# Kernel tuning notes

Measured on AMD Instinct MI355X. Metric: run time of the kernel, lower is better.

The kernel has to match this reference:

```python
import jax, jax.numpy as jnp
import numpy as np

D_IN = 1024
D_OUT = 1024
BATCH = 4
SEQ = 2048


def setup_inputs() -> dict:
    key = jax.random.key(0)
    kx, kq, kk, kv = jax.random.split(key, 4)
    # nn.Linear default init: U(-1/sqrt(d_in), 1/sqrt(d_in)); exact dist irrelevant for a reference
    bound = 1.0 / np.sqrt(D_IN)
    x = jax.random.normal(kx, (BATCH, SEQ, D_IN), dtype=jnp.float32)
    W_query = jax.random.uniform(kq, (D_IN, D_OUT), dtype=jnp.float32, minval=-bound, maxval=bound)
    W_key = jax.random.uniform(kk, (D_IN, D_OUT), dtype=jnp.float32, minval=-bound, maxval=bound)
    W_value = jax.random.uniform(kv, (D_IN, D_OUT), dtype=jnp.float32, minval=-bound, maxval=bound)
    return {"x": x, "W_query": W_query, "W_key": W_key, "W_value": W_value}


def reference(x, W_query, W_key, W_value):
    # x: [b, s, d_in]; projections (qkv_bias=False)
    q = jnp.einsum("bsd,df->bsf", x, W_query)  # [b, s, d_out]
    k = jnp.einsum("bsd,df->bsf", x, W_key)
    v = jnp.einsum("bsd,df->bsf", x, W_value)

    scale = 1.0 / jnp.sqrt(jnp.asarray(k.shape[-1], dtype=x.dtype))
    scores = jnp.einsum("bqf,bkf->bqk", q, k) * scale  # [b, s, s]

    s = x.shape[1]
    causal = jnp.tril(jnp.ones((s, s), dtype=bool))  # True where allowed
    scores = jnp.where(causal[None, :, :], scores, -jnp.inf)

    weights = jax.nn.softmax(scores, axis=-1)
    # dropout_ratio=0.0 -> identity
    return jnp.einsum("bqk,bkf->bqf", weights, v)  # [b, s, d_out]
```

## Files before the change

### kernel.cpp

```cpp
#include <hip/hip_runtime.h>


typedef __bf16 bf16x8 __attribute__((ext_vector_type(8)));
typedef float f32x4 __attribute__((ext_vector_type(4)));

__device__ __forceinline__ unsigned short f2bf(float f) {
  unsigned int u = __builtin_bit_cast(unsigned int, f);
  u += 0x7FFFu + ((u >> 16) & 1u);
  return (unsigned short)(u >> 16);
}
__device__ __forceinline__ float bf2f(unsigned short h) {
  unsigned int u = ((unsigned int)h) << 16;
  return __builtin_bit_cast(float, u);
}

#define GLDS16(g, l)                                                                   \
  __builtin_amdgcn_global_load_lds((const __attribute__((address_space(1))) void*)(g), \
                                   (__attribute__((address_space(3))) void*)(l), 16, 0, 0)

__global__ __launch_bounds__(256) void k_cvt(const float* __restrict__ in,
                                             unsigned short* __restrict__ out, long n) {
  long i = ((long)blockIdx.x * 256 + threadIdx.x) * 8;
  if (i >= n) return;
  float4 a = *(const float4*)(in + i);
  float4 b = *(const float4*)(in + i + 4);
  uint4 o;
  o.x = (unsigned)f2bf(a.x) | ((unsigned)f2bf(a.y) << 16);
  o.y = (unsigned)f2bf(a.z) | ((unsigned)f2bf(a.w) << 16);
  o.z = (unsigned)f2bf(b.x) | ((unsigned)f2bf(b.y) << 16);
  o.w = (unsigned)f2bf(b.z) | ((unsigned)f2bf(b.w) << 16);
  *(uint4*)(out + i) = o;
}

__global__ void k_trans_w(const float* __restrict__ W0, const float* __restrict__ W1,
                          const float* __restrict__ W2, unsigned short* __restrict__ Wt, int D) {
  const float* W = blockIdx.z == 0 ? W0 : (blockIdx.z == 1 ? W1 : W2);
  unsigned short* out = Wt + (long)blockIdx.z * D * D;
  __shared__ float tile[32][33];
  int tx = threadIdx.x, ty = threadIdx.y;
  int bx = blockIdx.x * 32, by = blockIdx.y * 32;
#pragma unroll
  for (int j = 0; j < 4; ++j) tile[ty + j * 8][tx] = W[(long)(by + ty + j * 8) * D + bx + tx];
  __syncthreads();
#pragma unroll
  for (int j = 0; j < 4; ++j)
    out[(long)(bx + ty + j * 8) * D + by + tx] = f2bf(tile[tx][ty + j * 8]);
}

template <typename CT>
__global__ __launch_bounds__(512, 2) void k_gemm256(const unsigned short* __restrict__ A,
                                                    const unsigned short* __restrict__ B,
                                                    CT* __restrict__ C, int nx, int ny, int N,
                                                    int K, long sA, long sB, long sC,
                                                    float alpha) {
  const unsigned bid = blockIdx.x;
  const unsigned cpx = gridDim.x >> 3;
  const unsigned logical = (bid & 7) * cpx + (bid >> 3);
  const int per_z = nx * ny;
  const int z = (int)(logical / per_z);
  const int rem = (int)(logical - (unsigned)z * per_z);
  const int by = rem / nx;
  const int bx = rem - by * nx;
  const int m0 = by * 256, n0 = bx * 256;
  A += (long)z * sA;
  B += (long)z * sB;
  C += (long)z * sC;

  __shared__ char lds[131072];

  const int t = threadIdx.x;
  const int l = t & 63;
  const int w = t >> 6;
  const int wm = w >> 2;
  const int wn = w & 3;

  const int srow = t >> 3;
  const int sch = (t & 7) ^ (srow & 7);
  const int soff = t * 16;

#define STG(mat, bf, hf, kt)                                                              \
  do {                                                                                    \
    const unsigned short* g =                                                             \
        ((mat) ? B + (long)(n0 + (hf)*128 + srow) * K : A + (long)(m0 + (hf)*128 + srow) * K) + \
        (long)(kt)*64 + sch * 8;                                                          \
    char* d = lds + (mat)*65536 + (bf)*32768 + (hf)*16384 + soff;                         \
    GLDS16(g, d);                                                                         \
    GLDS16(g + (long)64 * K, d + 8192);                                                   \
  } while (0)

  const int lx = l & 15;
  const int kx0 = ((l >> 4) ^ (l & 7)) * 16;
  const int kx1 = ((4 + (l >> 4)) ^ (l & 7)) * 16;
  char* const aB = lds + wm * 16384 + lx * 128;
  char* const bB = lds + 65536 + (wn >> 1) * 16384 + ((wn & 1) * 64 + lx) * 128;

  bf16x8 av[4][2], bv0[2][2], bv1[2][2];
  f32x4 acc[8][4];
#pragma unroll
  for (int i = 0; i < 8; ++i)
#pragma unroll
    for (int jn = 0; jn < 4; ++jn) acc[i][jn] = f32x4{0.f, 0.f, 0.f, 0.f};

#define RDA(bf, mh)                                                     \
  do {                                                                  \
    _Pragma("unroll") for (int m4 = 0; m4 < 4; ++m4) {                  \
      char* p = aB + (bf)*32768 + ((mh)*64 + m4 * 16) * 128;            \
      av[m4][0] = *(const bf16x8*)(p + kx0);                            \
      av[m4][1] = *(const bf16x8*)(p + kx1);                            \
    }                                                                   \
  } while (0)
#define RDB(dst, bf, nh)                                                \
  do {                                                                  \
    _Pragma("unroll") for (int n2 = 0; n2 < 2; ++n2) {                  \
      char* p = bB + (bf)*32768 + (((nh)*2 + n2) * 16) * 128;           \
      dst[n2][0] = *(const bf16x8*)(p + kx0);                           \
      dst[n2][1] = *(const bf16x8*)(p + kx1);                           \
    }                                                                   \
  } while (0)
#define MFM(bv, mh, nh)                                                                    \
  do {                                                                                     \
    __builtin_amdgcn_s_setprio(1);                                                         \
    _Pragma("unroll") for (int m4 = 0; m4 < 4; ++m4) _Pragma("unroll") for (int n2 = 0;    \
                                                                            n2 < 2; ++n2) { \
      acc[(mh)*4 + m4][(nh)*2 + n2] = __builtin_amdgcn_mfma_f32_16x16x32_bf16(             \
          av[m4][0], bv[n2][0], acc[(mh)*4 + m4][(nh)*2 + n2], 0, 0, 0);                   \
      acc[(mh)*4 + m4][(nh)*2 + n2] = __builtin_amdgcn_mfma_f32_16x16x32_bf16(             \
          av[m4][1], bv[n2][1], acc[(mh)*4 + m4][(nh)*2 + n2], 0, 0, 0);                   \
    }                                                                                      \
    __builtin_amdgcn_s_setprio(0);                                                         \
  } while (0)
#define BAR __builtin_amdgcn_s_barrier()
#define VMC(n) asm volatile("s_waitcnt vmcnt(" #n ")" ::: "memory")

  const int KT = K >> 6;
  const int NIT = KT >> 1;

  STG(0, 0, 0, 0); STG(0, 0, 1, 0); STG(1, 0, 0, 0); STG(1, 0, 1, 0);
  STG(1, 1, 0, 1); STG(1, 1, 1, 1); STG(0, 1, 0, 1);
  VMC(6);
  BAR;

  for (int j = 0; j < NIT; ++j) {
    const bool full = (j < NIT - 1);
    RDA(0, 0); RDB(bv0, 0, 0);
    STG(0, 1, 1, 2 * j + 1);
    BAR; MFM(bv0, 0, 0); BAR;
    RDB(bv1, 0, 1);
    BAR; MFM(bv1, 0, 1); BAR;
    RDA(0, 1);
    if (full) STG(1, 0, 0, 2 * j + 2);
    BAR; MFM(bv1, 1, 1); BAR;
    if (full) {
      STG(0, 0, 0, 2 * j + 2); STG(1, 0, 1, 2 * j + 2);
      VMC(6);
    } else {
      VMC(0);
    }
    BAR; MFM(bv0, 1, 0); BAR;
    RDA(1, 0); RDB(bv0, 1, 0);
    if (full) STG(0, 0, 1, 2 * j + 2);
    BAR; MFM(bv0, 0, 0); BAR;
    RDB(bv1, 1, 1);
    BAR; MFM(bv1, 0, 1); BAR;
    RDA(1, 1);
    if (full) STG(1, 1, 0, 2 * j + 3);
    BAR; MFM(bv1, 1, 1); BAR;
    if (full) {
      STG(1, 1, 1, 2 * j + 3); STG(0, 1, 0, 2 * j + 3);
      VMC(6);
    }
    BAR; MFM(bv0, 1, 0); BAR;
  }

  const int rb = m0 + wm * 128 + (l >> 4) * 4;
  const int cb = n0 + wn * 64 + (l & 15);
#pragma unroll
  for (int m = 0; m < 8; ++m)
#pragma unroll
    for (int n = 0; n < 4; ++n)
#pragma unroll
      for (int i = 0; i < 4; ++i) {
        float v = acc[m][n][i] * alpha;
        long off = (long)(rb + m * 16 + i) * N + (cb + n * 16);
        if constexpr (sizeof(CT) == 2)
          C[off] = f2bf(v);
        else
          C[off] = v;
      }
#undef STG
#undef RDA
#undef RDB
#undef MFM
#undef BAR
#undef VMC
}

template <typename CT, int MODE>
__global__ __launch_bounds__(256) void k_gemm_bt(const unsigned short* __restrict__ A,
                                                 const unsigned short* __restrict__ B,
                                                 CT* __restrict__ C, int nx, int ny, int N, int K,
                                                 long sA, long sB, long sC, float alpha) {
  const unsigned bid = blockIdx.x;
  const unsigned cpx = gridDim.x >> 3;
  const unsigned logical = (bid & 7) * cpx + (bid >> 3);
  int z, by, bx;
  if constexpr (MODE == 1) {
    const int per_z = ny * (ny + 1) / 2;
    z = (int)(logical / per_z);
    int r = (int)(logical - (unsigned)z * per_z);
    int b = (int)((sqrtf(8.f * (float)r + 1.f) - 1.f) * 0.5f);
    while ((b + 1) * (b + 2) / 2 <= r) ++b;
    while (b * (b + 1) / 2 > r) --b;
    by = b;
    bx = r - b * (b + 1) / 2;
  } else {
    const int per_z = nx * ny;
    z = (int)(logical / per_z);
    int r = (int)(logical - (unsigned)z * per_z);
    int j = r / nx;
    bx = r - j * nx;
    by = (MODE == 2) ? ((j & 1) ? (ny - 1 - (j >> 1)) : (j >> 1)) : j;
  }
  const int m0 = by * 128;
  const int n0 = bx * 128;
  A += (long)z * sA;
  B += (long)z * sB;
  C += (long)z * sC;

  __shared__ unsigned short As[128 * 64];
  __shared__ unsigned short Bs[128 * 64];
  char* const AsB = (char*)As;
  char* const BsB = (char*)Bs;

  const int t = threadIdx.x;
  const int l = t & 63;
  const int w = t >> 6;
  const int wr = (w >> 1) * 64;
  const int wc = (w & 1) * 64;

  const int srow = t >> 3;
  const int sch = (t & 7) ^ (srow & 7);
  const unsigned short* Ag = A + (long)(m0 + srow) * K + sch * 8;
  const unsigned short* Bg = B + (long)(n0 + srow) * K + sch * 8;
  const int soff = t * 16;

  const int ar = wr + (l & 15);
  const int brr = wc + (l & 15);
  const int kc = l >> 4;

  f32x4 acc[4][4];
#pragma unroll
  for (int i = 0; i < 4; ++i)
#pragma unroll
    for (int j = 0; j < 4; ++j) acc[i][j] = f32x4{0.f, 0.f, 0.f, 0.f};

  int KT = K >> 6;
  if (MODE == 2) {
    int kt2 = (m0 + 128) >> 6;
    KT = KT < kt2 ? KT : kt2;
  }

  for (int kt = 0; kt < KT; ++kt) {
    const long ko = (long)kt * 64;
#pragma unroll
    for (int i = 0; i < 4; ++i) GLDS16(Ag + (long)i * 32 * K + ko, AsB + i * 4096 + soff);
#pragma unroll
    for (int i = 0; i < 4; ++i) GLDS16(Bg + (long)i * 32 * K + ko, BsB + i * 4096 + soff);
    __syncthreads();
#pragma unroll
    for (int kk = 0; kk < 2; ++kk) {
      bf16x8 av[4], bv[4];
#pragma unroll
      for (int m = 0; m < 4; ++m) {
        int r = ar + m * 16;
        int c = (kk * 4 + kc) ^ (r & 7);
        av[m] = *(const bf16x8*)(AsB + r * 128 + c * 16);
      }
#pragma unroll
      for (int n = 0; n < 4; ++n) {
        int r = brr + n * 16;
        int c = (kk * 4 + kc) ^ (r & 7);
        bv[n] = *(const bf16x8*)(BsB + r * 128 + c * 16);
      }
#pragma unroll
      for (int m = 0; m < 4; ++m)
#pragma unroll
        for (int n = 0; n < 4; ++n)
          acc[m][n] = __builtin_amdgcn_mfma_f32_16x16x32_bf16(av[m], bv[n], acc[m][n], 0, 0, 0);
    }
    __syncthreads();
  }

  const int rb = m0 + wr + (l >> 4) * 4;
  const int cb = n0 + wc + (l & 15);
#pragma unroll
  for (int m = 0; m < 4; ++m)
#pragma unroll
    for (int n = 0; n < 4; ++n)
#pragma unroll
      for (int i = 0; i < 4; ++i) {
        float v = acc[m][n][i] * alpha;
        long off = (long)(rb + m * 16 + i) * N + (cb + n * 16);
        if constexpr (sizeof(CT) == 2)
          C[off] = f2bf(v);
        else
          C[off] = v;
      }
}

__global__ __launch_bounds__(256) void k_softmax(unsigned short* __restrict__ P, int S) {
  const int t = threadIdx.x;
  const int wv = t >> 6, l = t & 63;
  const int q = blockIdx.x * 4 + wv;
  unsigned short* row = P + ((long)blockIdx.y * S + q) * S;
  const int nch = (q >> 9) + 1;

  uint4 raw[4];
  float v[32];
#pragma unroll
  for (int j = 0; j < 4; ++j)
    if (j < nch) raw[j] = ((const uint4*)row)[j * 64 + l];
#pragma unroll
  for (int j = 0; j < 4; ++j) {
    if (j < nch) {
      unsigned int rw[4] = {raw[j].x, raw[j].y, raw[j].z, raw[j].w};
#pragma unroll
      for (int e = 0; e < 8; ++e)
        v[j * 8 + e] = bf2f((unsigned short)((rw[e >> 1] >> ((e & 1) * 16)) & 0xFFFF));
    }
  }

  float mx = -3.0e38f;
#pragma unroll
  for (int j = 0; j < 4; ++j)
    if (j < nch) {
#pragma unroll
      for (int e = 0; e < 8; ++e) {
        int col = j * 512 + l * 8 + e;
        if (col <= q) mx = fmaxf(mx, v[j * 8 + e]);
      }
    }
#pragma unroll
  for (int o = 32; o >= 1; o >>= 1) mx = fmaxf(mx, __shfl_xor(mx, o, 64));

  float s = 0.f;
#pragma unroll
  for (int j = 0; j < 4; ++j)
    if (j < nch) {
#pragma unroll
      for (int e = 0; e < 8; ++e) {
        int col = j * 512 + l * 8 + e;
        float ev = (col <= q) ? __expf(v[j * 8 + e] - mx) : 0.f;
        v[j * 8 + e] = ev;
        s += ev;
      }
    }
#pragma unroll
  for (int o = 32; o >= 1; o >>= 1) s += __shfl_xor(s, o, 64);
  const float inv = 1.f / s;

#pragma unroll
  for (int j = 0; j < 4; ++j)
    if (j < nch) {
      uint4 ow;
      unsigned int o2[4];
#pragma unroll
      for (int jj = 0; jj < 4; ++jj)
        o2[jj] = (unsigned)f2bf(v[j * 8 + 2 * jj] * inv) |
                 ((unsigned)f2bf(v[j * 8 + 2 * jj + 1] * inv) << 16);
      ow.x = o2[0]; ow.y = o2[1]; ow.z = o2[2]; ow.w = o2[3];
      ((uint4*)row)[j * 64 + l] = ow;
    }
}

extern "C" void kernel_launch(void* const* d_in, const int* in_sizes, int n_in, void* d_out,
                              int out_size, void* d_ws, size_t ws_size, hipStream_t stream) {
  const int B = 4, S = 2048, D = 1024;
  const long MS = (long)B * S;

  const float* x = (const float*)d_in[0];
  const float* Wq = (const float*)d_in[1];
  const float* Wk = (const float*)d_in[2];
  const float* Wv = (const float*)d_in[3];
  float* out = (float*)d_out;

  unsigned short* xb = (unsigned short*)d_ws;
  unsigned short* Wt = xb + MS * D;
  unsigned short* Qb = Wt + 3L * D * D;
  unsigned short* Kb = Qb + MS * D;
  unsigned short* Vt = Kb + MS * D;
  unsigned short* P  = Vt + MS * D;
  (void)ws_size;

  long n = MS * D;
  k_cvt<<<dim3((unsigned)(n / 8 / 256)), 256, 0, stream>>>(x, xb, n);
  k_trans_w<<<dim3(32, 32, 3), dim3(32, 8), 0, stream>>>(Wq, Wk, Wv, Wt, D);
  k_gemm256<unsigned short><<<256, 512, 0, stream>>>(
      xb, Wt, Qb, D / 256, (int)(MS / 256), D, D,
      0L, (long)D * D, MS * D, 1.0f);
  k_gemm_bt<unsigned short, 0><<<512, 256, 0, stream>>>(
      Wt + 2L * D * D, xb, Vt, S / 128, D / 128, S, D,
      0L, (long)S * D, (long)D * S, 1.0f);
  k_gemm_bt<unsigned short, 1><<<544, 256, 0, stream>>>(
      Qb, Kb, P, S / 128, S / 128, S, D,
      (long)S * D, (long)S * D, (long)S * S, 0.03125f);
  k_softmax<<<dim3(S / 4, B), 256, 0, stream>>>(P, S);
  k_gemm_bt<float, 2><<<512, 256, 0, stream>>>(
      P, Vt, out, D / 128, S / 128, D, S,
      (long)S * S, (long)D * S, (long)S * D, 1.0f);
}
```

Measured before the change: 153.5 us.

## Use 128x64 tiles with causal row-pair balancing for score and PV GEMMs

Adds a k_gemm_bt64 kernel with 128x64 output tiles. The QK^T score GEMM launches 1088 blocks over a finer lower-triangular tile map to cut wasted upper-triangle work. The PV GEMM pairs row-block by with 15-by in each block, so every block does the same total causal K-length and load is balanced. This trades larger tiles (more reuse per load) for more blocks and even work across CUs, with per-block B reuse lower.

```diff
diff --git a/kernel.cpp b/kernel.cpp
--- a/kernel.cpp
+++ b/kernel.cpp
@@ -195,7 +195,7 @@
 #undef VMC
 }
 
-template <typename CT, int MODE>
+template <typename CT>
 __global__ __launch_bounds__(256) void k_gemm_bt(const unsigned short* __restrict__ A,
                                                  const unsigned short* __restrict__ B,
                                                  CT* __restrict__ C, int nx, int ny, int N, int K,
@@ -203,24 +203,11 @@
   const unsigned bid = blockIdx.x;
   const unsigned cpx = gridDim.x >> 3;
   const unsigned logical = (bid & 7) * cpx + (bid >> 3);
-  int z, by, bx;
-  if constexpr (MODE == 1) {
-    const int per_z = ny * (ny + 1) / 2;
-    z = (int)(logical / per_z);
-    int r = (int)(logical - (unsigned)z * per_z);
-    int b = (int)((sqrtf(8.f * (float)r + 1.f) - 1.f) * 0.5f);
-    while ((b + 1) * (b + 2) / 2 <= r) ++b;
-    while (b * (b + 1) / 2 > r) --b;
-    by = b;
-    bx = r - b * (b + 1) / 2;
-  } else {
-    const int per_z = nx * ny;
-    z = (int)(logical / per_z);
-    int r = (int)(logical - (unsigned)z * per_z);
-    int j = r / nx;
-    bx = r - j * nx;
-    by = (MODE == 2) ? ((j & 1) ? (ny - 1 - (j >> 1)) : (j >> 1)) : j;
-  }
+  const int per_z = nx * ny;
+  const int z = (int)(logical / per_z);
+  const int r = (int)(logical - (unsigned)z * per_z);
+  const int by = r / nx;
+  const int bx = r - by * nx;
   const int m0 = by * 128;
   const int n0 = bx * 128;
   A += (long)z * sA;
@@ -254,12 +241,7 @@
 #pragma unroll
     for (int j = 0; j < 4; ++j) acc[i][j] = f32x4{0.f, 0.f, 0.f, 0.f};
 
-  int KT = K >> 6;
-  if (MODE == 2) {
-    int kt2 = (m0 + 128) >> 6;
-    KT = KT < kt2 ? KT : kt2;
-  }
-
+  const int KT = K >> 6;
   for (int kt = 0; kt < KT; ++kt) {
     const long ko = (long)kt * 64;
 #pragma unroll
@@ -272,15 +254,15 @@
       bf16x8 av[4], bv[4];
 #pragma unroll
       for (int m = 0; m < 4; ++m) {
-        int r = ar + m * 16;
-        int c = (kk * 4 + kc) ^ (r & 7);
-        av[m] = *(const bf16x8*)(AsB + r * 128 + c * 16);
+        int rr = ar + m * 16;
+        int c = (kk * 4 + kc) ^ (rr & 7);
+        av[m] = *(const bf16x8*)(AsB + rr * 128 + c * 16);
       }
 #pragma unroll
       for (int n = 0; n < 4; ++n) {
-        int r = brr + n * 16;
-        int c = (kk * 4 + kc) ^ (r & 7);
-        bv[n] = *(const bf16x8*)(BsB + r * 128 + c * 16);
+        int rr = brr + n * 16;
+        int c = (kk * 4 + kc) ^ (rr & 7);
+        bv[n] = *(const bf16x8*)(BsB + rr * 128 + c * 16);
       }
 #pragma unroll
       for (int m = 0; m < 4; ++m)
@@ -308,6 +290,120 @@
       }
 }
 
+template <typename CT, int MODE>
+__global__ __launch_bounds__(256) void k_gemm_bt64(const unsigned short* __restrict__ A,
+                                                   const unsigned short* __restrict__ B,
+                                                   CT* __restrict__ C, int N, int K, long sA,
+                                                   long sB, long sC, float alpha) {
+  const unsigned bid = blockIdx.x;
+  const unsigned cpx = gridDim.x >> 3;
+  const unsigned logical = (bid & 7) * cpx + (bid >> 3);
+  int z, by, bx;
+  if constexpr (MODE == 0) {
+    const int per_z = 272;
+    z = (int)(logical / per_z);
+    int r = (int)(logical - (unsigned)z * per_z);
+    int b = (int)((sqrtf(4.f * (float)r + 1.f) - 1.f) * 0.5f);
+    while ((b + 1) * (b + 2) <= r) ++b;
+    while (b * (b + 1) > r) --b;
+    by = b;
+    bx = r - b * (b + 1);
+  } else {
+    const int nx = N >> 6;
+    const int per_z = 8 * nx;
+    z = (int)(logical / per_z);
+    int r = (int)(logical - (unsigned)z * per_z);
+    by = r / nx;
+    bx = r - by * nx;
+  }
+  A += (long)z * sA;
+  B += (long)z * sB;
+  C += (long)z * sC;
+
+  __shared__ unsigned short As[128 * 64];
+  __shared__ unsigned short Bs[64 * 64];
+  char* const AsB = (char*)As;
+  char* const BsB = (char*)Bs;
+
+  const int t = threadIdx.x;
+  const int l = t & 63;
+  const int w = t >> 6;
+  const int wr = (w >> 1) * 64;
+  const int wc = (w & 1) * 32;
+
+  const int srow = t >> 3;
+  const int sch = (t & 7) ^ (srow & 7);
+  const int soff = t * 16;
+
+  const int ar = wr + (l & 15);
+  const int brr = wc + (l & 15);
+  const int kc = l >> 4;
+
+  const int n0 = bx * 64;
+  const unsigned short* Bg = B + (long)(n0 + srow) * K + sch * 8;
+
+  const int nseg = (MODE == 1) ? 2 : 1;
+  for (int seg = 0; seg < nseg; ++seg) {
+    const int row = (MODE == 1) ? (seg ? (15 - by) : by) : by;
+    const int m0 = row * 128;
+    const int KT = (MODE == 1) ? ((m0 + 128) >> 6) : (K >> 6);
+    const unsigned short* Ag = A + (long)(m0 + srow) * K + sch * 8;
+
+    f32x4 acc[4][2];
+#pragma unroll
+    for (int i = 0; i < 4; ++i)
+#pragma unroll
+      for (int j = 0; j < 2; ++j) acc[i][j] = f32x4{0.f, 0.f, 0.f, 0.f};
+
+    for (int kt = 0; kt < KT; ++kt) {
+      const long ko = (long)kt * 64;
+#pragma unroll
+      for (int i = 0; i < 4; ++i) GLDS16(Ag + (long)i * 32 * K + ko, AsB + i * 4096 + soff);
+#pragma unroll
+      for (int i = 0; i < 2; ++i) GLDS16(Bg + (long)i * 32 * K + ko, BsB + i * 4096 + soff);
+      __syncthreads();
+#pragma unroll
+      for (int kk = 0; kk < 2; ++kk) {
+        bf16x8 av[4], bv[2];
+#pragma unroll
+        for (int m = 0; m < 4; ++m) {
+          int rr = ar + m * 16;
+          int c = (kk * 4 + kc) ^ (rr & 7);
+          av[m] = *(const bf16x8*)(AsB + rr * 128 + c * 16);
+        }
+#pragma unroll
+        for (int n = 0; n < 2; ++n) {
+          int rr = brr + n * 16;
+          int c = (kk * 4 + kc) ^ (rr & 7);
+          bv[n] = *(const bf16x8*)(BsB + rr * 128 + c * 16);
+        }
+#pragma unroll
+        for (int m = 0; m < 4; ++m)
+#pragma unroll
+          for (int n = 0; n < 2; ++n)
+            acc[m][n] = __builtin_amdgcn_mfma_f32_16x16x32_bf16(av[m], bv[n], acc[m][n], 0, 0, 0);
+      }
+      __syncthreads();
+    }
+
+    const int rb = m0 + wr + (l >> 4) * 4;
+    const int cb = n0 + wc + (l & 15);
+#pragma unroll
+    for (int m = 0; m < 4; ++m)
+#pragma unroll
+      for (int n = 0; n < 2; ++n)
+#pragma unroll
+        for (int i = 0; i < 4; ++i) {
+          float v = acc[m][n][i] * alpha;
+          long off = (long)(rb + m * 16 + i) * N + (cb + n * 16);
+          if constexpr (sizeof(CT) == 2)
+            C[off] = f2bf(v);
+          else
+            C[off] = v;
+        }
+  }
+}
+
 __global__ __launch_bounds__(256) void k_softmax(unsigned short* __restrict__ P, int S) {
   const int t = threadIdx.x;
   const int wv = t >> 6, l = t & 63;
@@ -398,14 +494,14 @@
   k_gemm256<unsigned short><<<256, 512, 0, stream>>>(
       xb, Wt, Qb, D / 256, (int)(MS / 256), D, D,
       0L, (long)D * D, MS * D, 1.0f);
-  k_gemm_bt<unsigned short, 0><<<512, 256, 0, stream>>>(
+  k_gemm_bt<unsigned short><<<512, 256, 0, stream>>>(
       Wt + 2L * D * D, xb, Vt, S / 128, D / 128, S, D,
       0L, (long)S * D, (long)D * S, 1.0f);
-  k_gemm_bt<unsigned short, 1><<<544, 256, 0, stream>>>(
-      Qb, Kb, P, S / 128, S / 128, S, D,
+  k_gemm_bt64<unsigned short, 0><<<1088, 256, 0, stream>>>(
+      Qb, Kb, P, S, D,
       (long)S * D, (long)S * D, (long)S * S, 0.03125f);
   k_softmax<<<dim3(S / 4, B), 256, 0, stream>>>(P, S);
-  k_gemm_bt<float, 2><<<512, 256, 0, stream>>>(
-      P, Vt, out, D / 128, S / 128, D, S,
+  k_gemm_bt64<float, 1><<<512, 256, 0, stream>>>(
+      P, Vt, out, D, S,
       (long)S * S, (long)D * S, (long)S * D, 1.0f);
 }
```

Measured after the change: 145.3 us. 1.06x faster.
